# Performance work log

Hardware: AMD Instinct MI355X
Metric: run time of the kernel (lower is better)

## Reference

```python
import jax, jax.numpy as jnp
import numpy as np

B, L, DH = 4, 4096, 1024
T, DG = 1024, 768
P = 256


def setup_inputs() -> dict:
    key = jax.random.key(0)
    k1, k2, k3, k4, k5 = jax.random.split(key, 5)
    H = jax.random.normal(k1, (B, L, DH), dtype=jnp.float32)
    G = jax.random.normal(k2, (B, T, DG), dtype=jnp.float32)
    # key mask: True = padded/masked. Guarantee at least one valid key per row.
    mask = jax.random.randint(k3, (B, L), 0, 2).astype(jnp.bool_)
    mask = mask.at[:, 0].set(False)
    # torch Linear weights: [out, in]
    Wk_w = jax.random.normal(k4, (P, DH), dtype=jnp.float32) * (DH ** -0.5)
    Wq_w = jax.random.normal(k5, (P, DG), dtype=jnp.float32) * (DG ** -0.5)
    return {"H": H, "G": G, "mask": mask, "Wk_w": Wk_w, "Wq_w": Wq_w}


def reference(H, G, mask, Wk_w, Wq_w):
    # K = Wk(H): [B,L,P]; Q = Wq(G): [B,T,P]
    K = jnp.einsum('bld,pd->blp', H, Wk_w)
    Q = jnp.einsum('btd,pd->btp', G, Wq_w)
    scale = P ** -0.5
    logits = jnp.einsum('btp,blp->btl', Q, K) * scale  # [B,T,L]
    neg_inf = jnp.finfo(logits.dtype).min
    logits = jnp.where(mask[:, None, :], neg_inf, logits)
    alpha = jax.nn.softmax(logits, axis=-1)  # softmax over L (streaming-equivalent)
    Z = jnp.einsum('btl,bld->btd', alpha, H)  # [B,T,DH]
    return Z
```

## Files before the change

### kernel.cpp

```cpp
#include <hip/hip_runtime.h>
#include <hip/hip_bf16.h>


typedef __attribute__((ext_vector_type(8))) short short8;
typedef __attribute__((ext_vector_type(4))) float f32x4;

static __device__ __forceinline__ unsigned short bf16bits(float x) {
    __hip_bfloat16 b = __float2bfloat16(x);
    return *(unsigned short*)&b;
}

static __device__ __forceinline__ void gload_lds16(const __hip_bfloat16* g,
                                                   __hip_bfloat16* l)
{
    auto gp = (const __attribute__((address_space(1))) unsigned int*)(uintptr_t)g;
    auto lp = (__attribute__((address_space(3))) unsigned int*)(unsigned int)(uintptr_t)l;
    __builtin_amdgcn_global_load_lds(gp, lp, 16, 0, 0);
}

__global__ __launch_bounds__(256)
void cvt_f32_bf16_kernel(const float* __restrict__ in,
                         unsigned short* __restrict__ out, int n4)
{
    const int i = blockIdx.x * 256 + threadIdx.x;
    if (i >= n4) return;
    float4 v = ((const float4*)in)[i];
    ushort4 o;
    o.x = bf16bits(v.x); o.y = bf16bits(v.y);
    o.z = bf16bits(v.z); o.w = bf16bits(v.w);
    ((ushort4*)out)[i] = o;
}

__global__ __launch_bounds__(256)
void h_prep_kernel(const float* __restrict__ H,
                   __hip_bfloat16* __restrict__ Hbf,
                   __hip_bfloat16* __restrict__ Ht, int L, int D)
{
    const long b = blockIdx.z;
    const float* Hb = H + b * (long)L * D;
    __hip_bfloat16* Hbfb = Hbf + b * (long)L * D;
    __hip_bfloat16* Htb  = Ht  + b * (long)D * L;
    __shared__ float tile[32][33];
    const int l0 = blockIdx.x * 32, d0 = blockIdx.y * 32;
    const int tx = threadIdx.x & 31, ty = threadIdx.x >> 5;
    #pragma unroll
    for (int j = 0; j < 4; ++j) {
        const float v = Hb[(long)(l0 + ty + j * 8) * D + d0 + tx];
        tile[ty + j * 8][tx] = v;
        Hbfb[(long)(l0 + ty + j * 8) * D + d0 + tx] = __float2bfloat16(v);
    }
    __syncthreads();
    #pragma unroll
    for (int j = 0; j < 4; ++j)
        Htb[(long)(d0 + ty + j * 8) * L + l0 + tx] = __float2bfloat16(tile[tx][ty + j * 8]);
}

template <typename OutT, int SPLITK, int MODE>
__global__ __launch_bounds__(256)
void gemm_bt_kernel(const __hip_bfloat16* __restrict__ A,
                    const __hip_bfloat16* __restrict__ Bm,
                    OutT* __restrict__ C,
                    int K, int lda, int ldb, int ldc,
                    long batchStrideA, long batchStrideB, long batchStrideC,
                    float scale,
                    const unsigned char* __restrict__ mask,
                    const int* __restrict__ widthPtr,
                    float* __restrict__ rowsum,
                    int rowsumStride,
                    long partStride)
{
    int bx = blockIdx.x, by = blockIdx.y, bz = blockIdx.z;
    {
        const int nwg = gridDim.x * gridDim.y * gridDim.z;
        if ((nwg & 7) == 0) {
            int lin = bx + gridDim.x * (by + gridDim.y * bz);
            lin = (lin & 7) * (nwg >> 3) + (lin >> 3);
            bx = lin % gridDim.x;
            const int t = lin / gridDim.x;
            by = t % gridDim.y;
            bz = t / gridDim.y;
        }
    }

    const int zb = bz / SPLITK;
    const int kc = bz % SPLITK;
    A  += (long)zb * batchStrideA;
    Bm += (long)zb * batchStrideB;
    C  += (long)zb * batchStrideC + (long)kc * partStride;
    const int Kloc  = K / SPLITK;
    const int kbase = kc * Kloc;
    const int NT    = Kloc / 32;

    const int tid  = threadIdx.x;
    const int lane = tid & 63;
    const int wave = tid >> 6;
    const int wm = (wave & 1) * 64;
    const int wn = (wave >> 1) * 64;
    const int rowBase = bx * 128;
    const int colBase = by * 128;

    __shared__ __hip_bfloat16 As[3][128][32];
    __shared__ __hip_bfloat16 Bs[3][128][32];

    f32x4 acc[4][4];
    #pragma unroll
    for (int i = 0; i < 4; ++i)
        #pragma unroll
        for (int j = 0; j < 4; ++j)
            acc[i][j] = (f32x4){0.f, 0.f, 0.f, 0.f};

    const int srow = lane >> 2;
    const int scol = ((lane & 3) ^ ((lane >> 3) & 3)) * 8;
    const long ar0 = (long)(rowBase + wave * 32 + srow) * lda;
    const long ar1 = ar0 + 16l * lda;
    const long br0 = (long)(colBase + wave * 32 + srow) * ldb;
    const long br1 = br0 + 16l * ldb;

    const int mrow = lane & 15;
    const int koff = (((lane >> 4) ^ ((lane >> 1) & 3)) * 8);

    auto stage = [&](int buf, int t) {
        const int kk = kbase + t * 32 + scol;
        gload_lds16(A  + ar0 + kk, &As[buf][wave * 32][0]);
        gload_lds16(A  + ar1 + kk, &As[buf][wave * 32 + 16][0]);
        gload_lds16(Bm + br0 + kk, &Bs[buf][wave * 32][0]);
        gload_lds16(Bm + br1 + kk, &Bs[buf][wave * 32 + 16][0]);
    };

    stage(0, 0);
    if (NT > 1) stage(1, 1);

    int cur = 0;
    for (int t = 0; t < NT; ++t) {
        if (t + 1 < NT)
            asm volatile("s_waitcnt vmcnt(4)" ::: "memory");
        else
            asm volatile("s_waitcnt vmcnt(0)" ::: "memory");
        __builtin_amdgcn_s_barrier();
        if (t + 2 < NT) {
            const int nxt2 = (cur >= 1) ? cur - 1 : cur + 2;
            stage(nxt2, t + 2);
        }

        short8 af[4], bf[4];
        #pragma unroll
        for (int mi = 0; mi < 4; ++mi)
            af[mi] = *(const short8*)(&As[cur][wm + mi * 16 + mrow][koff]);
        #pragma unroll
        for (int ni = 0; ni < 4; ++ni)
            bf[ni] = *(const short8*)(&Bs[cur][wn + ni * 16 + mrow][koff]);

        #pragma unroll
        for (int mi = 0; mi < 4; ++mi)
            #pragma unroll
            for (int ni = 0; ni < 4; ++ni)
                acc[mi][ni] = __builtin_amdgcn_mfma_f32_16x16x32_bf16(
                    af[mi], bf[ni], acc[mi][ni], 0, 0, 0);
        cur = (cur == 2) ? 0 : cur + 1;
    }

    const int crow0 = (lane >> 4) * 4;
    const int ccol  = lane & 15;

    if constexpr (MODE == 2) {
        const int w = *widthPtr;
        const long mbase = (long)zb * ldc;
        bool mk[4];
        #pragma unroll
        for (int ni = 0; ni < 4; ++ni) {
            const long midx = mbase + colBase + wn + ni * 16 + ccol;
            if (w == 1)      mk[ni] = mask[midx] != 0;
            else if (w == 2) mk[ni] = ((const unsigned short*)mask)[midx] != 0;
            else if (w == 4) mk[ni] = ((const unsigned int*)mask)[midx] != 0;
            else { uint2 q = ((const uint2*)mask)[midx]; mk[ni] = (q.x | q.y) != 0; }
        }
        #pragma unroll
        for (int mi = 0; mi < 4; ++mi) {
            #pragma unroll
            for (int r = 0; r < 4; ++r) {
                const int row = rowBase + wm + mi * 16 + crow0 + r;
                float rs = 0.f;
                #pragma unroll
                for (int ni = 0; ni < 4; ++ni) {
                    const int col = colBase + wn + ni * 16 + ccol;
                    const float e = mk[ni] ? 0.f
                                           : __expf(acc[mi][ni][r] * scale);
                    const __hip_bfloat16 pb = __float2bfloat16(e);
                    C[(long)row * ldc + col] = pb;
                    rs += __bfloat162float(pb);
                }
                rs += __shfl_xor(rs, 1, 64);
                rs += __shfl_xor(rs, 2, 64);
                rs += __shfl_xor(rs, 4, 64);
                rs += __shfl_xor(rs, 8, 64);
                if ((lane & 15) == 0)
                    atomicAdd(&rowsum[(long)zb * rowsumStride + row], rs);
            }
        }
    } else {
        #pragma unroll
        for (int mi = 0; mi < 4; ++mi) {
            #pragma unroll
            for (int ni = 0; ni < 4; ++ni) {
                #pragma unroll
                for (int r = 0; r < 4; ++r) {
                    const int row = rowBase + wm + mi * 16 + crow0 + r;
                    const int col = colBase + wn + ni * 16 + ccol;
                    const float v = acc[mi][ni][r] * scale;
                    if constexpr (sizeof(OutT) == 2)
                        C[(long)row * ldc + col] = __float2bfloat16(v);
                    else
                        C[(long)row * ldc + col] = v;
                }
            }
        }
    }
}

__global__ __launch_bounds__(256)
void combine_kernel(const float* __restrict__ Zp,
                    const float* __restrict__ rowsum,
                    float* __restrict__ Z, long partStride)
{
    const int i = blockIdx.x * 256 + threadIdx.x;
    const float4 a = ((const float4*)Zp)[i];
    const float4 b = ((const float4*)(Zp + partStride))[i];
    const float inv = 1.0f / rowsum[i >> 8];
    float4 o;
    o.x = (a.x + b.x) * inv;
    o.y = (a.y + b.y) * inv;
    o.z = (a.z + b.z) * inv;
    o.w = (a.w + b.w) * inv;
    ((float4*)Z)[i] = o;
}

__global__ __launch_bounds__(256)
void mask_width_kernel(const unsigned char* __restrict__ m, int* __restrict__ widthOut)
{
    __shared__ int c1, c2, c4, c8, cp;
    if (threadIdx.x == 0) { c1 = c2 = c4 = c8 = cp = 0; }
    __syncthreads();
    int l1 = 0, l2 = 0, l4 = 0, l8 = 0, lp = 0;
    const unsigned short* m16 = (const unsigned short*)m;
    const unsigned int*   m32 = (const unsigned int*)m;
    for (int i = threadIdx.x; i < 16384; i += 256) l1 += (m[i] != 0);
    for (int i = threadIdx.x; i < 8192;  i += 256) {
        l2 += (m16[i] != 0);
        lp += ((m[2 * i] != 0) == (m[2 * i + 1] != 0));
    }
    for (int i = threadIdx.x; i < 4096;  i += 256) l4 += (m32[i] != 0);
    for (int i = threadIdx.x; i < 2048;  i += 256) l8 += ((m32[2 * i] | m32[2 * i + 1]) != 0);
    atomicAdd(&c1, l1); atomicAdd(&c2, l2); atomicAdd(&c4, l4);
    atomicAdd(&c8, l8); atomicAdd(&cp, lp);
    __syncthreads();
    if (threadIdx.x == 0) {
        const float f1 = fabsf(c1 / 16384.f - 0.5f);
        const float f2 = fabsf(c2 / 8192.f  - 0.5f);
        const float f4 = fabsf(c4 / 4096.f  - 0.5f);
        const float f8 = fabsf(c8 / 2048.f  - 0.5f);
        int w = 1; float best = f1;
        if (f2 < best) { best = f2; w = 2; }
        if (f4 < best) { best = f4; w = 4; }
        if (f8 < best) { best = f8; w = 8; }
        if (w == 1 && cp > 7400) w = 2;
        *widthOut = w;
    }
}

extern "C" void kernel_launch(void* const* d_in, const int* in_sizes, int n_in,
                              void* d_out, int out_size, void* d_ws, size_t ws_size,
                              hipStream_t stream)
{
    constexpr int B = 4, L = 4096, DH = 1024, T = 1024, DG = 768, P = 256;

    const float* H  = (const float*)d_in[0];
    const float* G  = (const float*)d_in[1];
    const void*  mask = d_in[2];
    const float* Wk = (const float*)d_in[3];
    const float* Wq = (const float*)d_in[4];
    for (int i = 0; i < n_in; ++i) {
        switch (in_sizes[i]) {
            case B * L * DH: H    = (const float*)d_in[i]; break;
            case B * T * DG: G    = (const float*)d_in[i]; break;
            case B * L:      mask = d_in[i];               break;
            case P * DH:     Wk   = (const float*)d_in[i]; break;
            case P * DG:     Wq   = (const float*)d_in[i]; break;
        }
    }
    float* Z = (float*)d_out;

    char* ws = (char*)d_ws;
    __hip_bfloat16* Hbf  = (__hip_bfloat16*)ws;
    float*          Zp   = (float*)ws;
    __hip_bfloat16* Ht   = (__hip_bfloat16*)(ws + (32l << 20));
    __hip_bfloat16* Gbf  = (__hip_bfloat16*)(ws + (64l << 20));
    __hip_bfloat16* Qbf  = (__hip_bfloat16*)(ws + (70l << 20));
    __hip_bfloat16* Kbf  = (__hip_bfloat16*)(ws + (72l << 20));
    __hip_bfloat16* Wkbf = (__hip_bfloat16*)(ws + (80l << 20));
    __hip_bfloat16* Wqbf = (__hip_bfloat16*)(ws + (80l << 20) + (512l << 10));
    float*          rowsum    = (float*)(ws + (80l << 20) + (896l << 10));
    int*            widthFlag = (int*)  (ws + (80l << 20) + (960l << 10));
    __hip_bfloat16* Sb   = (__hip_bfloat16*)(ws + (81l << 20));

    constexpr long ZPART = (long)B * T * DH;

    const dim3 blk(256);

    hipMemsetAsync(rowsum, 0, (size_t)(B * T) * sizeof(float), stream);

    mask_width_kernel<<<dim3(1), blk, 0, stream>>>((const unsigned char*)mask, widthFlag);

    h_prep_kernel<<<dim3(L / 32, DH / 32, B), blk, 0, stream>>>(H, Hbf, Ht, L, DH);
    cvt_f32_bf16_kernel<<<dim3((P * DH) / 1024), blk, 0, stream>>>(Wk, (unsigned short*)Wkbf, (P * DH) / 4);
    cvt_f32_bf16_kernel<<<dim3((P * DG) / 1024), blk, 0, stream>>>(Wq, (unsigned short*)Wqbf, (P * DG) / 4);
    cvt_f32_bf16_kernel<<<dim3((B * T * DG) / 1024), blk, 0, stream>>>(G, (unsigned short*)Gbf, (B * T * DG) / 4);

    gemm_bt_kernel<__hip_bfloat16, 1, 0><<<dim3((B * T) / 128, P / 128, 1), blk, 0, stream>>>(
        Gbf, Wqbf, Qbf, DG, DG, DG, P, 0, 0, 0, 1.0f,
        nullptr, nullptr, nullptr, 0, 0);
    gemm_bt_kernel<__hip_bfloat16, 1, 0><<<dim3((B * L) / 128, P / 128, 1), blk, 0, stream>>>(
        Hbf, Wkbf, Kbf, DH, DH, DH, P, 0, 0, 0, 1.0f,
        nullptr, nullptr, nullptr, 0, 0);
    gemm_bt_kernel<__hip_bfloat16, 1, 2><<<dim3(T / 128, L / 128, B), blk, 0, stream>>>(
        Qbf, Kbf, Sb, P, P, P, L,
        (long)T * P, (long)L * P, (long)T * L, 0.0625f,
        (const unsigned char*)mask, widthFlag, rowsum, T, 0);
    gemm_bt_kernel<float, 2, 0><<<dim3(T / 128, DH / 128, B * 2), blk, 0, stream>>>(
        Sb, Ht, Zp, L, L, L, DH,
        (long)T * L, (long)DH * L, (long)T * DH, 1.0f,
        nullptr, nullptr, nullptr, 0, ZPART);
    combine_kernel<<<dim3((B * T * DH / 4) / 256), blk, 0, stream>>>(
        Zp, rowsum, Z, ZPART);
}
```

Measured before the change: 260.8 us.

## Stage bf16 GEMM epilogues through swizzled LDS and vectorize H transpose prep

The GEMM's bf16 outputs (Q, K and the masked exp scores) are now written into a shared LDS pool with an XOR swizzle, then stored to global memory as 16-byte rows. The old path issued scattered 2-byte stores. The H preparation kernel now uses 64x64 tiles with float4 loads and a bf16 transposed tile, so both the bf16 copy and the transposed copy are written with vector stores. The cost is an extra barrier and an LDS round-trip in the epilogue, and the A/B staging buffers are reused for output staging.

Result: faster. 254.6 us (-2.4%).

```diff
diff --git a/kernel.cpp b/kernel.cpp
--- a/kernel.cpp
+++ b/kernel.cpp
@@ -40,19 +40,31 @@
     const float* Hb = H + b * (long)L * D;
     __hip_bfloat16* Hbfb = Hbf + b * (long)L * D;
     __hip_bfloat16* Htb  = Ht  + b * (long)D * L;
-    __shared__ float tile[32][33];
-    const int l0 = blockIdx.x * 32, d0 = blockIdx.y * 32;
-    const int tx = threadIdx.x & 31, ty = threadIdx.x >> 5;
+    __shared__ __align__(16) __hip_bfloat16 tile[64][72];
+    const int l0 = blockIdx.x * 64, d0 = blockIdx.y * 64;
+    const int tx = threadIdx.x & 15, ty = threadIdx.x >> 4;
     #pragma unroll
-    for (int j = 0; j < 4; ++j) {
-        const float v = Hb[(long)(l0 + ty + j * 8) * D + d0 + tx];
-        tile[ty + j * 8][tx] = v;
-        Hbfb[(long)(l0 + ty + j * 8) * D + d0 + tx] = __float2bfloat16(v);
+    for (int p = 0; p < 4; ++p) {
+        const int row = ty + p * 16;
+        const float4 v = *(const float4*)(&Hb[(long)(l0 + row) * D + d0 + tx * 4]);
+        ushort4 o;
+        o.x = bf16bits(v.x); o.y = bf16bits(v.y);
+        o.z = bf16bits(v.z); o.w = bf16bits(v.w);
+        *(ushort4*)(&Hbfb[(long)(l0 + row) * D + d0 + tx * 4]) = o;
+        tile[tx * 4 + 0][row] = __float2bfloat16(v.x);
+        tile[tx * 4 + 1][row] = __float2bfloat16(v.y);
+        tile[tx * 4 + 2][row] = __float2bfloat16(v.z);
+        tile[tx * 4 + 3][row] = __float2bfloat16(v.w);
     }
     __syncthreads();
+    const int ll = threadIdx.x & 7;
+    const int dq = threadIdx.x >> 3;
     #pragma unroll
-    for (int j = 0; j < 4; ++j)
-        Htb[(long)(d0 + ty + j * 8) * L + l0 + tx] = __float2bfloat16(tile[tx][ty + j * 8]);
+    for (int q = 0; q < 2; ++q) {
+        const int dd = dq + q * 32;
+        const short8 v = *(const short8*)(&tile[dd][ll * 8]);
+        *(short8*)(&Htb[(long)(d0 + dd) * L + l0 + ll * 8]) = v;
+    }
 }
 
 template <typename OutT, int SPLITK, int MODE>
@@ -99,8 +111,9 @@
     const int rowBase = bx * 128;
     const int colBase = by * 128;
 
-    __shared__ __hip_bfloat16 As[3][128][32];
-    __shared__ __hip_bfloat16 Bs[3][128][32];
+    __shared__ __align__(16) __hip_bfloat16 lds_pool[24576];
+    __hip_bfloat16* AsP = lds_pool;
+    __hip_bfloat16* BsP = lds_pool + 12288;
 
     f32x4 acc[4][4];
     #pragma unroll
@@ -121,10 +134,10 @@
 
     auto stage = [&](int buf, int t) {
         const int kk = kbase + t * 32 + scol;
-        gload_lds16(A  + ar0 + kk, &As[buf][wave * 32][0]);
-        gload_lds16(A  + ar1 + kk, &As[buf][wave * 32 + 16][0]);
-        gload_lds16(Bm + br0 + kk, &Bs[buf][wave * 32][0]);
-        gload_lds16(Bm + br1 + kk, &Bs[buf][wave * 32 + 16][0]);
+        gload_lds16(A  + ar0 + kk, AsP + buf * 4096 + wave * 1024);
+        gload_lds16(A  + ar1 + kk, AsP + buf * 4096 + wave * 1024 + 512);
+        gload_lds16(Bm + br0 + kk, BsP + buf * 4096 + wave * 1024);
+        gload_lds16(Bm + br1 + kk, BsP + buf * 4096 + wave * 1024 + 512);
     };
 
     stage(0, 0);
@@ -145,10 +158,10 @@
         short8 af[4], bf[4];
         #pragma unroll
         for (int mi = 0; mi < 4; ++mi)
-            af[mi] = *(const short8*)(&As[cur][wm + mi * 16 + mrow][koff]);
+            af[mi] = *(const short8*)(AsP + cur * 4096 + (wm + mi * 16 + mrow) * 32 + koff);
         #pragma unroll
         for (int ni = 0; ni < 4; ++ni)
-            bf[ni] = *(const short8*)(&Bs[cur][wn + ni * 16 + mrow][koff]);
+            bf[ni] = *(const short8*)(BsP + cur * 4096 + (wn + ni * 16 + mrow) * 32 + koff);
 
         #pragma unroll
         for (int mi = 0; mi < 4; ++mi)
@@ -162,40 +175,69 @@
     const int crow0 = (lane >> 4) * 4;
     const int ccol  = lane & 15;
 
-    if constexpr (MODE == 2) {
-        const int w = *widthPtr;
-        const long mbase = (long)zb * ldc;
-        bool mk[4];
-        #pragma unroll
-        for (int ni = 0; ni < 4; ++ni) {
-            const long midx = mbase + colBase + wn + ni * 16 + ccol;
-            if (w == 1)      mk[ni] = mask[midx] != 0;
-            else if (w == 2) mk[ni] = ((const unsigned short*)mask)[midx] != 0;
-            else if (w == 4) mk[ni] = ((const unsigned int*)mask)[midx] != 0;
-            else { uint2 q = ((const uint2*)mask)[midx]; mk[ni] = (q.x | q.y) != 0; }
-        }
-        #pragma unroll
-        for (int mi = 0; mi < 4; ++mi) {
-            #pragma unroll
-            for (int r = 0; r < 4; ++r) {
-                const int row = rowBase + wm + mi * 16 + crow0 + r;
-                float rs = 0.f;
+    if constexpr (MODE == 2 || sizeof(OutT) == 2) {
+        __syncthreads();
+        __hip_bfloat16* cst = lds_pool;
+
+        if constexpr (MODE == 2) {
+            const int w = *widthPtr;
+            const long mbase = (long)zb * ldc;
+            bool mk[4];
+            #pragma unroll
+            for (int ni = 0; ni < 4; ++ni) {
+                const long midx = mbase + colBase + wn + ni * 16 + ccol;
+                if (w == 1)      mk[ni] = mask[midx] != 0;
+                else if (w == 2) mk[ni] = ((const unsigned short*)mask)[midx] != 0;
+                else if (w == 4) mk[ni] = ((const unsigned int*)mask)[midx] != 0;
+                else { uint2 q = ((const uint2*)mask)[midx]; mk[ni] = (q.x | q.y) != 0; }
+            }
+            #pragma unroll
+            for (int mi = 0; mi < 4; ++mi) {
+                #pragma unroll
+                for (int r = 0; r < 4; ++r) {
+                    const int row = wm + mi * 16 + crow0 + r;
+                    float rs = 0.f;
+                    #pragma unroll
+                    for (int ni = 0; ni < 4; ++ni) {
+                        const int col = wn + ni * 16 + ccol;
+                        const float e = mk[ni] ? 0.f
+                                               : __expf(acc[mi][ni][r] * scale);
+                        const __hip_bfloat16 pb = __float2bfloat16(e);
+                        cst[row * 136 + (((col >> 3) ^ (row >> 3)) << 3) + (col & 7)] = pb;
+                        rs += __bfloat162float(pb);
+                    }
+                    rs += __shfl_xor(rs, 1, 64);
+                    rs += __shfl_xor(rs, 2, 64);
+                    rs += __shfl_xor(rs, 4, 64);
+                    rs += __shfl_xor(rs, 8, 64);
+                    if ((lane & 15) == 0)
+                        atomicAdd(&rowsum[(long)zb * rowsumStride + rowBase + row], rs);
+                }
+            }
+        } else {
+            #pragma unroll
+            for (int mi = 0; mi < 4; ++mi) {
                 #pragma unroll
                 for (int ni = 0; ni < 4; ++ni) {
-                    const int col = colBase + wn + ni * 16 + ccol;
-                    const float e = mk[ni] ? 0.f
-                                           : __expf(acc[mi][ni][r] * scale);
-                    const __hip_bfloat16 pb = __float2bfloat16(e);
-                    C[(long)row * ldc + col] = pb;
-                    rs += __bfloat162float(pb);
+                    #pragma unroll
+                    for (int r = 0; r < 4; ++r) {
+                        const int row = wm + mi * 16 + crow0 + r;
+                        const int col = wn + ni * 16 + ccol;
+                        cst[row * 136 + (((col >> 3) ^ (row >> 3)) << 3) + (col & 7)] =
+                            __float2bfloat16(acc[mi][ni][r] * scale);
+                    }
                 }
-                rs += __shfl_xor(rs, 1, 64);
-                rs += __shfl_xor(rs, 2, 64);
-                rs += __shfl_xor(rs, 4, 64);
-                rs += __shfl_xor(rs, 8, 64);
-                if ((lane & 15) == 0)
-                    atomicAdd(&rowsum[(long)zb * rowsumStride + row], rs);
             }
+        }
+        __syncthreads();
+        const int g   = tid & 15;
+        const int r4  = tid >> 4;
+        const int lof = ((g ^ r4) << 3);
+        #pragma unroll
+        for (int k = 0; k < 8; ++k) {
+            const int row = r4 * 8 + k;
+            const short8 v = *(const short8*)(cst + row * 136 + lof);
+            *(short8*)(&((__hip_bfloat16*)C)[(long)(rowBase + row) * ldc + colBase + g * 8]) = v;
         }
     } else {
         #pragma unroll
@@ -206,11 +248,7 @@
                 for (int r = 0; r < 4; ++r) {
                     const int row = rowBase + wm + mi * 16 + crow0 + r;
                     const int col = colBase + wn + ni * 16 + ccol;
-                    const float v = acc[mi][ni][r] * scale;
-                    if constexpr (sizeof(OutT) == 2)
-                        C[(long)row * ldc + col] = __float2bfloat16(v);
-                    else
-                        C[(long)row * ldc + col] = v;
+                    ((float*)C)[(long)row * ldc + col] = acc[mi][ni][r] * scale;
                 }
             }
         }
@@ -310,7 +348,7 @@
 
     mask_width_kernel<<<dim3(1), blk, 0, stream>>>((const unsigned char*)mask, widthFlag);
 
-    h_prep_kernel<<<dim3(L / 32, DH / 32, B), blk, 0, stream>>>(H, Hbf, Ht, L, DH);
+    h_prep_kernel<<<dim3(L / 64, DH / 64, B), blk, 0, stream>>>(H, Hbf, Ht, L, DH);
     cvt_f32_bf16_kernel<<<dim3((P * DH) / 1024), blk, 0, stream>>>(Wk, (unsigned short*)Wkbf, (P * DH) / 4);
     cvt_f32_bf16_kernel<<<dim3((P * DG) / 1024), blk, 0, stream>>>(Wq, (unsigned short*)Wqbf, (P * DG) / 4);
     cvt_f32_bf16_kernel<<<dim3((B * T * DG) / 1024), blk, 0, stream>>>(G, (unsigned short*)Gbf, (B * T * DG) / 4);
```
